# Optimization experiments

Measured on AMD Instinct MI355X. Metric: run time of the kernel, lower is better.

Reference implementation:

```python
import jax, jax.numpy as jnp
import numpy as np

KEEP_RATIO = 0.1
FS = 8          # feature_size
BN_EPS = 1e-5


def dct_matrix(N):
    # Orthonormal DCT-II matrix: D[k,n] = s_k * cos(pi*(2n+1)*k/(2N))
    n = jnp.arange(N, dtype=jnp.float32)
    k = n[:, None]
    D = jnp.cos(jnp.pi * (2.0 * n + 1.0) * k / (2.0 * N))
    scale = jnp.full((N, 1), jnp.sqrt(2.0 / N), jnp.float32).at[0, 0].set(jnp.sqrt(1.0 / N))
    return D * scale


def bilinear_resize(x, out_h, out_w):
    # torch F.interpolate bilinear, align_corners=False (half-pixel centers, no antialias)
    def coords(in_size, out):
        src = (jnp.arange(out, dtype=jnp.float32) + 0.5) * (in_size / out) - 0.5
        src = jnp.clip(src, 0.0, in_size - 1.0)
        i0 = jnp.floor(src).astype(jnp.int32)
        i1 = jnp.minimum(i0 + 1, in_size - 1)
        return i0, i1, src - i0.astype(jnp.float32)
    r0, r1, rw = coords(x.shape[2], out_h)
    c0, c1, cw = coords(x.shape[3], out_w)
    x = x[:, :, r0, :] * (1.0 - rw)[:, None] + x[:, :, r1, :] * rw[:, None]
    x = x[:, :, :, c0] * (1.0 - cw) + x[:, :, :, c1] * cw
    return x


def apply_dct(x):
    H, W = x.shape[2], x.shape[3]
    Dh, Dw = dct_matrix(H), dct_matrix(W)
    # 2D DCT-II (ortho): Y = Dh @ X @ Dw^T
    y = jnp.einsum('hi,bcij,wj->bchw', Dh, x, Dw)
    hk, wk = int(H * KEEP_RATIO), int(W * KEEP_RATIO)
    mask = jnp.zeros((H, W), x.dtype).at[:hk, :wk].set(1.0)  # low-pass keep top-left block
    y = y * mask
    # inverse DCT (ortho): X = Dh^T @ Y @ Dw
    x = jnp.einsum('ih,bchw,jw->bcij', Dh, y, Dw)
    return bilinear_resize(x, FS, FS)


def generate_gradient_image(x):
    # scipy convolve2d flips the kernel, but flipped sobel == -sobel and we take abs,
    # so plain correlation with sobel is equivalent. boundary='wrap' -> circular pad.
    sx = jnp.array([[-1, 0, 1], [-2, 0, 2], [-1, 0, 1]], jnp.float32)
    sy = jnp.array([[-1, -2, -1], [0, 0, 0], [1, 2, 1]], jnp.float32)
    kern = jnp.stack([sx, sy])[:, None]  # [2,1,3,3]
    B, C, H, W = x.shape
    xc = x.reshape(B * C, 1, H, W)
    xp = jnp.pad(xc, ((0, 0), (0, 0), (1, 1), (1, 1)), mode='wrap')
    g = jax.lax.conv_general_dilated(xp, kern, (1, 1), 'VALID')  # [B*C,2,H,W]
    grad = jnp.sqrt(g[:, 0] ** 2 + g[:, 1] ** 2).reshape(B, C, H, W)
    return bilinear_resize(grad, FS, FS)


def feature_extractor(x, w, b, gamma, beta):
    y = jax.lax.conv_general_dilated(x, w, (1, 1), ((1, 1), (1, 1)))
    y = y + b[None, :, None, None]
    # BatchNorm (inference: running_mean=0, running_var=1)
    y = y * (gamma / jnp.sqrt(1.0 + BN_EPS))[None, :, None, None] + beta[None, :, None, None]
    y = jax.nn.relu(y)
    # input is already FS x FS, so AdaptiveAvgPool2d((8,8)) is the identity
    return y


def setup_inputs() -> dict:
    key = jax.random.key(0)
    ks = jax.random.split(key, 10)
    B, C, H, W = 128, 3, 256, 256
    return {
        'x': jax.random.normal(ks[0], (B, C, H, W), jnp.float32),
        'conv_dct_w': jax.random.normal(ks[1], (64, 3, 3, 3), jnp.float32) * 0.1,
        'conv_dct_b': jnp.zeros((64,), jnp.float32),
        'bn_dct_g': jnp.ones((64,), jnp.float32),
        'bn_dct_b': jnp.zeros((64,), jnp.float32),
        'conv_grad_w': jax.random.normal(ks[2], (64, 3, 3, 3), jnp.float32) * 0.1,
        'conv_grad_b': jnp.zeros((64,), jnp.float32),
        'bn_grad_g': jnp.ones((64,), jnp.float32),
        'bn_grad_b': jnp.zeros((64,), jnp.float32),
        'fus_w': jax.random.normal(ks[3], (1, 64), jnp.float32) * 0.1,
        'fus_b': jnp.zeros((1,), jnp.float32),
        'cls_w': jax.random.normal(ks[4], (2, 64 * FS * FS), jnp.float32) * 0.02,
        'cls_b': jnp.zeros((2,), jnp.float32),
    }


def reference(x, conv_dct_w, conv_dct_b, bn_dct_g, bn_dct_b,
              conv_grad_w, conv_grad_b, bn_grad_g, bn_grad_b,
              fus_w, fus_b, cls_w, cls_b):
    dct_in = apply_dct(x)                       # [B,3,8,8]
    grad_in = generate_gradient_image(x)        # [B,3,8,8]
    d = feature_extractor(dct_in, conv_dct_w, conv_dct_b, bn_dct_g, bn_dct_b)    # [B,64,8,8]
    g = feature_extractor(grad_in, conv_grad_w, conv_grad_b, bn_grad_g, bn_grad_b)
    # FeatureFusion: weight = sigmoid(fc(avgpool(d+g)))
    s = jnp.mean(d + g, axis=(2, 3))            # [B,64]
    w = jax.nn.sigmoid(s @ fus_w.T + fus_b)     # [B,1]
    w = w[:, :, None, None]
    fused = w * d + (1.0 - w) * g               # [B,64,8,8]
    flat = fused.reshape(fused.shape[0], -1)
    return flat @ cls_w.T + cls_b               # [B,2]
```

## Files before the change

kernel.cpp:

```cpp
#include <hip/hip_runtime.h>
#include <math.h>


__global__ __launch_bounds__(256) void k_compute_E(float* __restrict__ E) {
    __shared__ float F[8][25];
    const int tid = threadIdx.x;
    const float c0 = 3.14159265358979323846f / 512.0f;
    if (tid < 25) {
        const int k = tid;
        const float scale = (k == 0) ? sqrtf(1.0f / 256.0f) : sqrtf(2.0f / 256.0f);
        for (int p = 0; p < 8; ++p) {
            const int r0 = 32 * p + 15;
            const float a = cosf(c0 * (float)((2 * r0 + 1) * k));
            const float b = cosf(c0 * (float)((2 * r0 + 3) * k));
            F[p][k] = 0.5f * (a + b) * scale;
        }
    }
    __syncthreads();
    const int j = tid;
    float acc[8] = {0.f, 0.f, 0.f, 0.f, 0.f, 0.f, 0.f, 0.f};
    for (int k = 0; k < 25; ++k) {
        const float scale = (k == 0) ? sqrtf(1.0f / 256.0f) : sqrtf(2.0f / 256.0f);
        const float Dkj = cosf(c0 * (float)((2 * j + 1) * k)) * scale;
        #pragma unroll
        for (int p = 0; p < 8; ++p) acc[p] = fmaf(F[p][k], Dkj, acc[p]);
    }
    for (int p = 0; p < 8; ++p) E[p * 256 + j] = acc[p];
}

__global__ __launch_bounds__(512) void k_dct(const float* __restrict__ x,
                                             const float* __restrict__ Eg,
                                             float* __restrict__ dct_out) {
    __shared__ float El[8][257];
    __shared__ float T[8][257];
    const int img = blockIdx.x;
    const float* xi = x + (size_t)img * 65536;
    const int tid = threadIdx.x;
    const int j = tid & 255;
    const int half = tid >> 8;

    for (int idx = tid; idx < 2048; idx += 512) El[idx >> 8][idx & 255] = Eg[idx];
    __syncthreads();

    float t[8] = {0.f, 0.f, 0.f, 0.f, 0.f, 0.f, 0.f, 0.f};
    const int i0 = half * 128;
    for (int i = i0; i < i0 + 128; ++i) {
        const float v = xi[i * 256 + j];
        #pragma unroll
        for (int p = 0; p < 8; ++p) t[p] = fmaf(El[p][i], v, t[p]);
    }
    if (half == 0) {
        #pragma unroll
        for (int p = 0; p < 8; ++p) T[p][j] = t[p];
    }
    __syncthreads();
    if (half == 1) {
        #pragma unroll
        for (int p = 0; p < 8; ++p) T[p][j] += t[p];
    }
    __syncthreads();
    if (tid < 64) {
        const int p = tid >> 3, q = tid & 7;
        float s = 0.0f;
        for (int jj = 0; jj < 256; ++jj) s = fmaf(T[p][jj], El[q][jj], s);
        dct_out[img * 64 + tid] = s;
    }
}

__global__ __launch_bounds__(64) void k_grad(const float* __restrict__ x,
                                             float* __restrict__ grad_out) {
    const int img = blockIdx.x;
    const int tid = threadIdx.x;
    const int p = tid >> 3, q = tid & 7;
    const float* xi = x + (size_t)img * 65536;
    const int r0 = 32 * p + 15, c0 = 32 * q + 15;
    float acc = 0.0f;
    #pragma unroll
    for (int dr = 0; dr < 2; ++dr) {
        #pragma unroll
        for (int dc = 0; dc < 2; ++dc) {
            const int r = r0 + dr, c = c0 + dc;
            const float a00 = xi[(r - 1) * 256 + (c - 1)];
            const float a01 = xi[(r - 1) * 256 + c];
            const float a02 = xi[(r - 1) * 256 + (c + 1)];
            const float a10 = xi[r * 256 + (c - 1)];
            const float a12 = xi[r * 256 + (c + 1)];
            const float a20 = xi[(r + 1) * 256 + (c - 1)];
            const float a21 = xi[(r + 1) * 256 + c];
            const float a22 = xi[(r + 1) * 256 + (c + 1)];
            const float gx = (a02 - a00) + 2.0f * (a12 - a10) + (a22 - a20);
            const float gy = (a20 - a00) + 2.0f * (a21 - a01) + (a22 - a02);
            acc += sqrtf(gx * gx + gy * gy);
        }
    }
    grad_out[img * 64 + tid] = 0.25f * acc;
}

__global__ __launch_bounds__(256) void k_head(
    const float* __restrict__ dct_in, const float* __restrict__ grad_in,
    const float* __restrict__ wd, const float* __restrict__ bd,
    const float* __restrict__ gd, const float* __restrict__ betad,
    const float* __restrict__ wg, const float* __restrict__ bg,
    const float* __restrict__ gg, const float* __restrict__ betag,
    const float* __restrict__ fus_w, const float* __restrict__ fus_b,
    const float* __restrict__ cls_w, const float* __restrict__ cls_b,
    float* __restrict__ out) {
    __shared__ float ind[3][8][8];
    __shared__ float ing[3][8][8];
    __shared__ float wdl[1728];
    __shared__ float wgl[1728];
    __shared__ float redS[256];
    __shared__ float redF[64];
    __shared__ float redO0[256];
    __shared__ float redO1[256];
    __shared__ float wshare;

    const int b = blockIdx.x;
    const int tid = threadIdx.x;
    const int co = tid & 63;
    const int chunk = tid >> 6;

    float* pind = &ind[0][0][0];
    float* ping = &ing[0][0][0];
    for (int i = tid; i < 192; i += 256) {
        pind[i] = dct_in[b * 192 + i];
        ping[i] = grad_in[b * 192 + i];
    }
    for (int i = tid; i < 1728; i += 256) {
        wdl[i] = wd[i];
        wgl[i] = wg[i];
    }
    __syncthreads();

    const float scale_d = gd[co] / sqrtf(1.0f + 1e-5f);
    const float scale_g = gg[co] / sqrtf(1.0f + 1e-5f);
    const float beta_d = betad[co];
    const float beta_g = betag[co];
    const float bias_d = bd[co];
    const float bias_g = bg[co];

    float dreg[16], greg[16];
    float ssum = 0.0f;
    int idx = 0;
    for (int pr = chunk * 2; pr < chunk * 2 + 2; ++pr) {
        for (int qc = 0; qc < 8; ++qc) {
            float sd = bias_d, sg = bias_g;
            for (int ci = 0; ci < 3; ++ci) {
                #pragma unroll
                for (int du = 0; du < 3; ++du) {
                    const int r = pr + du - 1;
                    if (r < 0 || r > 7) continue;
                    #pragma unroll
                    for (int dv = 0; dv < 3; ++dv) {
                        const int c = qc + dv - 1;
                        if (c < 0 || c > 7) continue;
                        const float wv_d = wdl[co * 27 + ci * 9 + du * 3 + dv];
                        const float wv_g = wgl[co * 27 + ci * 9 + du * 3 + dv];
                        sd = fmaf(wv_d, ind[ci][r][c], sd);
                        sg = fmaf(wv_g, ing[ci][r][c], sg);
                    }
                }
            }
            sd = fmaxf(sd * scale_d + beta_d, 0.0f);
            sg = fmaxf(sg * scale_g + beta_g, 0.0f);
            dreg[idx] = sd;
            greg[idx] = sg;
            ssum += sd + sg;
            ++idx;
        }
    }

    redS[tid] = ssum;
    __syncthreads();
    if (tid < 64) {
        const float s =
            (redS[co] + redS[64 + co] + redS[128 + co] + redS[192 + co]) *
            (1.0f / 64.0f);
        redF[co] = s * fus_w[co];
    }
    __syncthreads();
    if (tid == 0) {
        float z = fus_b[0];
        for (int i = 0; i < 64; ++i) z += redF[i];
        wshare = 1.0f / (1.0f + expf(-z));
    }
    __syncthreads();
    const float wgt = wshare;

    float po0 = 0.0f, po1 = 0.0f;
    idx = 0;
    for (int pr = chunk * 2; pr < chunk * 2 + 2; ++pr) {
        for (int qc = 0; qc < 8; ++qc) {
            const float f = wgt * dreg[idx] + (1.0f - wgt) * greg[idx];
            const int n = co * 64 + pr * 8 + qc;
            po0 = fmaf(f, cls_w[n], po0);
            po1 = fmaf(f, cls_w[4096 + n], po1);
            ++idx;
        }
    }
    redO0[tid] = po0;
    redO1[tid] = po1;
    __syncthreads();
    if (tid < 64) {
        redO0[tid] += redO0[tid + 64] + redO0[tid + 128] + redO0[tid + 192];
        redO1[tid] += redO1[tid + 64] + redO1[tid + 128] + redO1[tid + 192];
    }
    __syncthreads();
    if (tid == 0) {
        float s = cls_b[0];
        for (int i = 0; i < 64; ++i) s += redO0[i];
        out[b * 2 + 0] = s;
    }
    if (tid == 1) {
        float s = cls_b[1];
        for (int i = 0; i < 64; ++i) s += redO1[i];
        out[b * 2 + 1] = s;
    }
}

extern "C" void kernel_launch(void* const* d_in, const int* in_sizes, int n_in,
                              void* d_out, int out_size, void* d_ws, size_t ws_size,
                              hipStream_t stream) {
    const float* x     = (const float*)d_in[0];
    const float* wd    = (const float*)d_in[1];
    const float* bd    = (const float*)d_in[2];
    const float* gd    = (const float*)d_in[3];
    const float* betad = (const float*)d_in[4];
    const float* wg    = (const float*)d_in[5];
    const float* bg    = (const float*)d_in[6];
    const float* gg    = (const float*)d_in[7];
    const float* betag = (const float*)d_in[8];
    const float* fusw  = (const float*)d_in[9];
    const float* fusb  = (const float*)d_in[10];
    const float* clsw  = (const float*)d_in[11];
    const float* clsb  = (const float*)d_in[12];
    float* out = (float*)d_out;

    float* ws = (float*)d_ws;
    float* E       = ws;
    float* dct_in  = ws + 2048;
    float* grad_in = ws + 2048 + 24576;

    k_compute_E<<<1, 256, 0, stream>>>(E);
    k_grad<<<384, 64, 0, stream>>>(x, grad_in);
    k_dct<<<384, 512, 0, stream>>>(x, E, dct_in);
    k_head<<<128, 256, 0, stream>>>(dct_in, grad_in, wd, bd, gd, betad,
                                    wg, bg, gg, betag, fusw, fusb, clsw, clsb,
                                    out);
}
```

Measured before the change: 203.3 us.

## Transpose DCT projection matrix and vectorize DCT loads; parallelize gradient per sample

The precomputed projection matrix is now stored transposed (row-major by pixel) so each DCT thread reads 8 coefficients with two float4 shared loads and processes two columns via float2 global loads. The row range is split across four warp groups, with a serialized shared-memory accumulation, and the final 8x8 contraction is split across all 512 threads with a partial-sum reduction. The gradient kernel uses 256 threads, one per bilinear sample, combined with shuffles instead of one thread looping over four. The cosine argument computation is also restructured, which may slightly change numerics.

Measured after the change: 197.0 us. -3.1%, faster.

```diff
diff --git a/kernel.cpp b/kernel.cpp
--- a/kernel.cpp
+++ b/kernel.cpp
@@ -2,18 +2,18 @@
 #include <math.h>
 
 
-__global__ __launch_bounds__(256) void k_compute_E(float* __restrict__ E) {
+__global__ __launch_bounds__(256) void k_compute_Et(float* __restrict__ Et) {
     __shared__ float F[8][25];
     const int tid = threadIdx.x;
-    const float c0 = 3.14159265358979323846f / 512.0f;
+    const float pi_f = 3.14159274101257324f;
     if (tid < 25) {
         const int k = tid;
         const float scale = (k == 0) ? sqrtf(1.0f / 256.0f) : sqrtf(2.0f / 256.0f);
         for (int p = 0; p < 8; ++p) {
-            const int r0 = 32 * p + 15;
-            const float a = cosf(c0 * (float)((2 * r0 + 1) * k));
-            const float b = cosf(c0 * (float)((2 * r0 + 3) * k));
-            F[p][k] = 0.5f * (a + b) * scale;
+            const int n0 = 32 * p + 15;
+            const float a0 = (pi_f * (float)(2 * n0 + 1)) * (float)k / 512.0f;
+            const float a1 = (pi_f * (float)(2 * n0 + 3)) * (float)k / 512.0f;
+            F[p][k] = 0.5f * (cosf(a0) + cosf(a1)) * scale;
         }
     }
     __syncthreads();
@@ -21,79 +21,109 @@
     float acc[8] = {0.f, 0.f, 0.f, 0.f, 0.f, 0.f, 0.f, 0.f};
     for (int k = 0; k < 25; ++k) {
         const float scale = (k == 0) ? sqrtf(1.0f / 256.0f) : sqrtf(2.0f / 256.0f);
-        const float Dkj = cosf(c0 * (float)((2 * j + 1) * k)) * scale;
+        const float arg = (pi_f * (float)(2 * j + 1)) * (float)k / 512.0f;
+        const float Dkj = cosf(arg) * scale;
         #pragma unroll
         for (int p = 0; p < 8; ++p) acc[p] = fmaf(F[p][k], Dkj, acc[p]);
     }
-    for (int p = 0; p < 8; ++p) E[p * 256 + j] = acc[p];
+    #pragma unroll
+    for (int p = 0; p < 8; ++p) Et[j * 8 + p] = acc[p];
 }
 
 __global__ __launch_bounds__(512) void k_dct(const float* __restrict__ x,
-                                             const float* __restrict__ Eg,
+                                             const float* __restrict__ Etg,
                                              float* __restrict__ dct_out) {
-    __shared__ float El[8][257];
-    __shared__ float T[8][257];
+    __shared__ float Et[256][8];
+    __shared__ float T[8][256];
+    __shared__ float PO[8][64];
+
     const int img = blockIdx.x;
     const float* xi = x + (size_t)img * 65536;
     const int tid = threadIdx.x;
-    const int j = tid & 255;
-    const int half = tid >> 8;
-
-    for (int idx = tid; idx < 2048; idx += 512) El[idx >> 8][idx & 255] = Eg[idx];
-    __syncthreads();
-
-    float t[8] = {0.f, 0.f, 0.f, 0.f, 0.f, 0.f, 0.f, 0.f};
-    const int i0 = half * 128;
-    for (int i = i0; i < i0 + 128; ++i) {
-        const float v = xi[i * 256 + j];
-        #pragma unroll
-        for (int p = 0; p < 8; ++p) t[p] = fmaf(El[p][i], v, t[p]);
-    }
-    if (half == 0) {
-        #pragma unroll
-        for (int p = 0; p < 8; ++p) T[p][j] = t[p];
-    }
-    __syncthreads();
-    if (half == 1) {
-        #pragma unroll
-        for (int p = 0; p < 8; ++p) T[p][j] += t[p];
-    }
+
+    float* etf = &Et[0][0];
+    for (int i = tid; i < 2048; i += 512) etf[i] = Etg[i];
+    __syncthreads();
+
+    const int w = tid >> 6, l = tid & 63;
+    const int cw = w >> 1, ch = w & 1;
+    const int col = ch * 128 + 2 * l;
+
+    float acc[8][2];
+    #pragma unroll
+    for (int p = 0; p < 8; ++p) { acc[p][0] = 0.f; acc[p][1] = 0.f; }
+
+    const float* px = xi + (size_t)(cw * 64) * 256 + col;
+    #pragma unroll 4
+    for (int i = 0; i < 64; ++i) {
+        const float2 v = *(const float2*)px;
+        px += 256;
+        const int row = cw * 64 + i;
+        const float4 ea = *(const float4*)&Et[row][0];
+        const float4 eb = *(const float4*)&Et[row][4];
+        acc[0][0] = fmaf(ea.x, v.x, acc[0][0]); acc[0][1] = fmaf(ea.x, v.y, acc[0][1]);
+        acc[1][0] = fmaf(ea.y, v.x, acc[1][0]); acc[1][1] = fmaf(ea.y, v.y, acc[1][1]);
+        acc[2][0] = fmaf(ea.z, v.x, acc[2][0]); acc[2][1] = fmaf(ea.z, v.y, acc[2][1]);
+        acc[3][0] = fmaf(ea.w, v.x, acc[3][0]); acc[3][1] = fmaf(ea.w, v.y, acc[3][1]);
+        acc[4][0] = fmaf(eb.x, v.x, acc[4][0]); acc[4][1] = fmaf(eb.x, v.y, acc[4][1]);
+        acc[5][0] = fmaf(eb.y, v.x, acc[5][0]); acc[5][1] = fmaf(eb.y, v.y, acc[5][1]);
+        acc[6][0] = fmaf(eb.z, v.x, acc[6][0]); acc[6][1] = fmaf(eb.z, v.y, acc[6][1]);
+        acc[7][0] = fmaf(eb.w, v.x, acc[7][0]); acc[7][1] = fmaf(eb.w, v.y, acc[7][1]);
+    }
+
+    for (int r = 0; r < 4; ++r) {
+        if (cw == r) {
+            if (r == 0) {
+                #pragma unroll
+                for (int p = 0; p < 8; ++p) {
+                    float2 t; t.x = acc[p][0]; t.y = acc[p][1];
+                    *(float2*)&T[p][col] = t;
+                }
+            } else {
+                #pragma unroll
+                for (int p = 0; p < 8; ++p) {
+                    float2 t = *(const float2*)&T[p][col];
+                    t.x += acc[p][0]; t.y += acc[p][1];
+                    *(float2*)&T[p][col] = t;
+                }
+            }
+        }
+        __syncthreads();
+    }
+
+    const int pq = tid & 63, seg = tid >> 6;
+    const int p = pq >> 3, q = pq & 7;
+    float s = 0.0f;
+    const int j0 = seg * 32;
+    for (int j = j0; j < j0 + 32; ++j) s = fmaf(T[p][j], Et[j][q], s);
+    PO[seg][pq] = s;
     __syncthreads();
     if (tid < 64) {
-        const int p = tid >> 3, q = tid & 7;
-        float s = 0.0f;
-        for (int jj = 0; jj < 256; ++jj) s = fmaf(T[p][jj], El[q][jj], s);
-        dct_out[img * 64 + tid] = s;
-    }
-}
-
-__global__ __launch_bounds__(64) void k_grad(const float* __restrict__ x,
-                                             float* __restrict__ grad_out) {
+        float r = PO[0][tid] + PO[1][tid] + PO[2][tid] + PO[3][tid] +
+                  PO[4][tid] + PO[5][tid] + PO[6][tid] + PO[7][tid];
+        dct_out[img * 64 + tid] = r;
+    }
+}
+
+__global__ __launch_bounds__(256) void k_grad(const float* __restrict__ x,
+                                              float* __restrict__ grad_out) {
     const int img = blockIdx.x;
     const int tid = threadIdx.x;
-    const int p = tid >> 3, q = tid & 7;
+    const int s = tid & 3, pq = tid >> 2;
+    const int p = pq >> 3, q = pq & 7;
+    const int dr = s >> 1, dc = s & 1;
     const float* xi = x + (size_t)img * 65536;
-    const int r0 = 32 * p + 15, c0 = 32 * q + 15;
-    float acc = 0.0f;
-    #pragma unroll
-    for (int dr = 0; dr < 2; ++dr) {
-        #pragma unroll
-        for (int dc = 0; dc < 2; ++dc) {
-            const int r = r0 + dr, c = c0 + dc;
-            const float a00 = xi[(r - 1) * 256 + (c - 1)];
-            const float a01 = xi[(r - 1) * 256 + c];
-            const float a02 = xi[(r - 1) * 256 + (c + 1)];
-            const float a10 = xi[r * 256 + (c - 1)];
-            const float a12 = xi[r * 256 + (c + 1)];
-            const float a20 = xi[(r + 1) * 256 + (c - 1)];
-            const float a21 = xi[(r + 1) * 256 + c];
-            const float a22 = xi[(r + 1) * 256 + (c + 1)];
-            const float gx = (a02 - a00) + 2.0f * (a12 - a10) + (a22 - a20);
-            const float gy = (a20 - a00) + 2.0f * (a21 - a01) + (a22 - a02);
-            acc += sqrtf(gx * gx + gy * gy);
-        }
-    }
-    grad_out[img * 64 + tid] = 0.25f * acc;
+    const int r = 32 * p + 15 + dr, c = 32 * q + 15 + dc;
+    const float* base = xi + (r - 1) * 256 + (c - 1);
+    const float a00 = base[0],   a01 = base[1],   a02 = base[2];
+    const float a10 = base[256],                  a12 = base[258];
+    const float a20 = base[512], a21 = base[513], a22 = base[514];
+    const float gx = (a02 - a00) + 2.0f * (a12 - a10) + (a22 - a20);
+    const float gy = (a20 - a00) + 2.0f * (a21 - a01) + (a22 - a02);
+    float m = sqrtf(gx * gx + gy * gy);
+    m += __shfl_xor(m, 1);
+    m += __shfl_xor(m, 2);
+    if (s == 0) grad_out[img * 64 + pq] = 0.25f * m;
 }
 
 __global__ __launch_bounds__(256) void k_head(
@@ -237,13 +267,13 @@
     float* out = (float*)d_out;
 
     float* ws = (float*)d_ws;
-    float* E       = ws;
+    float* Et      = ws;
     float* dct_in  = ws + 2048;
     float* grad_in = ws + 2048 + 24576;
 
-    k_compute_E<<<1, 256, 0, stream>>>(E);
-    k_grad<<<384, 64, 0, stream>>>(x, grad_in);
-    k_dct<<<384, 512, 0, stream>>>(x, E, dct_in);
+    k_compute_Et<<<1, 256, 0, stream>>>(Et);
+    k_grad<<<384, 256, 0, stream>>>(x, grad_in);
+    k_dct<<<384, 512, 0, stream>>>(x, Et, dct_in);
     k_head<<<128, 256, 0, stream>>>(dct_in, grad_in, wd, bd, gd, betad,
                                     wg, bg, gg, betag, fusw, fusb, clsw, clsb,
                                     out);
```
